# Kernel optimization log

Measured on AMD Instinct MI355X. Metric: run time of the kernel, lower is better.

The kernel has to match this reference:

```python
import jax, jax.numpy as jnp
import numpy as np

B, C, H, W, R = 16, 64, 192, 192, 64

def setup_inputs() -> dict:
    key = jax.random.key(0)
    ks = jax.random.split(key, 8)
    return {
        "X":  jax.random.normal(ks[0], (B, C, H, W), dtype=jnp.float32),
        "p":  jnp.ones((R,), dtype=jnp.float32),  # parameter_r init = ones
        "Wc": jax.random.normal(ks[1], (R, C, C), dtype=jnp.float32) * (1.0 / np.sqrt(C)),
        "bc": jax.random.normal(ks[2], (R, C), dtype=jnp.float32) * 0.01,
        "Wh": jax.random.normal(ks[3], (R, H, H), dtype=jnp.float32) * (1.0 / np.sqrt(H)),
        "bh": jax.random.normal(ks[4], (R, H), dtype=jnp.float32) * 0.01,
        "Ww": jax.random.normal(ks[5], (R, W, W), dtype=jnp.float32) * (1.0 / np.sqrt(W)),
        "bw": jax.random.normal(ks[6], (R, W), dtype=jnp.float32) * 0.01,
    }

def reference(X, p, Wc, bc, Wh, bh, Ww, bw):
    # Global average pools (shared across all r iterations; the torch loop
    # recomputes them redundantly every iteration -- same values).
    cp = X.mean(axis=(2, 3))  # [B,C]  pool over H,W
    hp = X.mean(axis=(1, 3))  # [B,H]  pool over C,W (after permute 0,2,1,3)
    wp = X.mean(axis=(1, 2))  # [B,W]  pool over C,H (after permute 0,3,2,1)
    # Per-iteration 1x1 convs on [*,1,1] == batched affine maps, then sigmoid.
    Cw = jax.nn.sigmoid(jnp.einsum('rdc,bc->rbd', Wc, cp) + bc[:, None, :])  # [R,B,C]
    Hw = jax.nn.sigmoid(jnp.einsum('rdh,bh->rbd', Wh, hp) + bh[:, None, :])  # [R,B,H]
    Ww_ = jax.nn.sigmoid(jnp.einsum('rdw,bw->rbd', Ww, wp) + bw[:, None, :])  # [R,B,W]
    # y = sum_r p[r] * C_weight_r x H_weight_r x W_weight_r  (rank-1-per-axis outer)
    y = jnp.einsum('r,rbc,rbh,rbw->bchw', p, Cw, Hw, Ww_)
    return y * X
```

## Files before the change

kernel.cpp:

```cpp
#include <hip/hip_runtime.h>
#include <hip/hip_bf16.h>
#include <math.h>

#define B_  16
#define C_  64
#define H_  192
#define W_  192
#define R_  64
#define HW_ (H_*W_)

#define OFF_CP  0
#define OFF_HP  1024
#define OFF_WP  4096
#define OFF_MC  7168
#define OFF_HWS 72704
#define OFF_WWS 269312

typedef __attribute__((ext_vector_type(8))) short bf16x8;
typedef __attribute__((ext_vector_type(4))) float f32x4;

static __device__ __forceinline__ short f2bf(float f) {
    unsigned u = __float_as_uint(f);
    unsigned r = u + 0x7fffu + ((u >> 16) & 1u);
    return (short)(r >> 16);
}

__global__ __launch_bounds__(256) void zero_kernel(float* p, int n) {
    int i = blockIdx.x * 256 + threadIdx.x;
    if (i < n) p[i] = 0.f;
}

__global__ __launch_bounds__(256) void pool_kernel(const float* __restrict__ X,
                                                   float* __restrict__ cp,
                                                   float* __restrict__ hp,
                                                   float* __restrict__ wp) {
    int b = blockIdx.x >> 6;
    int c = blockIdx.x & 63;
    int tid = threadIdx.x;
    int wv = tid >> 6, lane = tid & 63;
    const float* base = X + (size_t)(b * C_ + c) * HW_ + wv * 48 * W_;

    __shared__ float rowsum[H_];
    __shared__ float colpart[4][W_];
    __shared__ float cpart[3];

    float col0 = 0.f, col1 = 0.f, col2 = 0.f;
    for (int hh = 0; hh < 48; hh += 4) {
        float x[4][3];
        #pragma unroll
        for (int u = 0; u < 4; ++u) {
            #pragma unroll
            for (int k = 0; k < 3; ++k)
                x[u][k] = base[(hh + u) * W_ + k * 64 + lane];
        }
        #pragma unroll
        for (int u = 0; u < 4; ++u) {
            col0 += x[u][0]; col1 += x[u][1]; col2 += x[u][2];
            float s = x[u][0] + x[u][1] + x[u][2];
            s += __shfl_down(s, 32);
            s += __shfl_down(s, 16);
            s += __shfl_down(s, 8);
            s += __shfl_down(s, 4);
            s += __shfl_down(s, 2);
            s += __shfl_down(s, 1);
            if (lane == 0) rowsum[wv * 48 + hh + u] = s;
        }
    }
    colpart[wv][lane]       = col0;
    colpart[wv][lane + 64]  = col1;
    colpart[wv][lane + 128] = col2;
    __syncthreads();

    const float inv_cw = 1.0f / 12288.0f;
    if (tid < 192) {
        float colv = colpart[0][tid] + colpart[1][tid] + colpart[2][tid] + colpart[3][tid];
        atomicAdd(&wp[b * W_ + tid], colv * inv_cw);
        float rv = rowsum[tid];
        atomicAdd(&hp[b * H_ + tid], rv * inv_cw);
        float s = rv;
        s += __shfl_down(s, 32);
        s += __shfl_down(s, 16);
        s += __shfl_down(s, 8);
        s += __shfl_down(s, 4);
        s += __shfl_down(s, 2);
        s += __shfl_down(s, 1);
        if ((tid & 63) == 0) cpart[tid >> 6] = s;
    }
    __syncthreads();
    if (tid == 0) cp[b * C_ + c] = (cpart[0] + cpart[1] + cpart[2]) * (1.0f / (float)HW_);
}

__global__ __launch_bounds__(256) void affine_sig_kernel(const float* __restrict__ Wsrc,
                                                         const float* __restrict__ bias,
                                                         const float* __restrict__ pool,
                                                         const float* __restrict__ p,
                                                         float* __restrict__ out,
                                                         int D, int K,
                                                         int s_b, int s_d, int s_r) {
    __shared__ float pl[16 * 193];
    int tid = threadIdx.x;
    for (int i = tid; i < 16 * K; i += 256) {
        int bb = i / K, kk = i - bb * K;
        pl[bb * (K + 1) + kk] = pool[i];
    }
    __syncthreads();

    int b  = tid & 15;
    int rl = tid >> 4;
    int row = blockIdx.x * 16 + rl;
    int r = row / D, d = row - r * D;

    const float4* w4 = (const float4*)(Wsrc + (size_t)row * K);
    const float*  pb = &pl[b * (K + 1)];
    float acc = 0.f;
    for (int k4 = 0; k4 < (K >> 2); ++k4) {
        float4 wv = w4[k4];
        int k = k4 << 2;
        acc += wv.x * pb[k] + wv.y * pb[k + 1] + wv.z * pb[k + 2] + wv.w * pb[k + 3];
    }
    acc += bias[row];
    float sgm = 1.0f / (1.0f + expf(-acc));
    if (p) sgm *= p[r];
    out[(size_t)b * s_b + (size_t)d * s_d + (size_t)r * s_r] = sgm;
}

__global__ __launch_bounds__(256) void main_kernel(const float* __restrict__ X,
                                                   const float* __restrict__ Mc,
                                                   const float* __restrict__ Hws,
                                                   const float* __restrict__ Wws,
                                                   float* __restrict__ out) {
    int blk = blockIdx.x;
    int b = blk / 576;
    int rem = blk - b * 576;
    int h = rem / 3;
    int w0 = (rem - h * 3) * 64;
    int tid = threadIdx.x;
    int wv = tid >> 6, lane = tid & 63;
    int m = lane & 15, quad = lane >> 4;
    int c0 = wv * 16;

    const float* McB = Mc + b * (C_ * R_);
    const float* HvB = Hws + ((size_t)b * H_ + h) * R_;
    const float* WwB = Wws + ((size_t)b * W_ + w0) * R_;

    bf16x8 afrag[2];
    float hv[2][8];
    #pragma unroll
    for (int ks = 0; ks < 2; ++ks) {
        const float4* ap = (const float4*)(McB + (c0 + m) * R_ + ks * 32 + quad * 8);
        const float4* hpp = (const float4*)(HvB + ks * 32 + quad * 8);
        float4 a0 = ap[0], a1 = ap[1];
        float4 h0 = hpp[0], h1 = hpp[1];
        afrag[ks][0] = f2bf(a0.x); afrag[ks][1] = f2bf(a0.y);
        afrag[ks][2] = f2bf(a0.z); afrag[ks][3] = f2bf(a0.w);
        afrag[ks][4] = f2bf(a1.x); afrag[ks][5] = f2bf(a1.y);
        afrag[ks][6] = f2bf(a1.z); afrag[ks][7] = f2bf(a1.w);
        hv[ks][0] = h0.x; hv[ks][1] = h0.y; hv[ks][2] = h0.z; hv[ks][3] = h0.w;
        hv[ks][4] = h1.x; hv[ks][5] = h1.y; hv[ks][6] = h1.z; hv[ks][7] = h1.w;
    }

    f32x4 acc[4];
    #pragma unroll
    for (int jt = 0; jt < 4; ++jt) acc[jt] = (f32x4){0.f, 0.f, 0.f, 0.f};

    #pragma unroll
    for (int jt = 0; jt < 4; ++jt) {
        #pragma unroll
        for (int ks = 0; ks < 2; ++ks) {
            const float4* bp = (const float4*)(WwB + (jt * 16 + m) * R_ + ks * 32 + quad * 8);
            float4 b0 = bp[0], b1 = bp[1];
            bf16x8 bfrag;
            bfrag[0] = f2bf(b0.x * hv[ks][0]); bfrag[1] = f2bf(b0.y * hv[ks][1]);
            bfrag[2] = f2bf(b0.z * hv[ks][2]); bfrag[3] = f2bf(b0.w * hv[ks][3]);
            bfrag[4] = f2bf(b1.x * hv[ks][4]); bfrag[5] = f2bf(b1.y * hv[ks][5]);
            bfrag[6] = f2bf(b1.z * hv[ks][6]); bfrag[7] = f2bf(b1.w * hv[ks][7]);
            acc[jt] = __builtin_amdgcn_mfma_f32_16x16x32_bf16(afrag[ks], bfrag, acc[jt], 0, 0, 0);
        }
    }

    size_t pixbase = (size_t)h * W_ + w0 + m;
    #pragma unroll
    for (int jt = 0; jt < 4; ++jt) {
        #pragma unroll
        for (int reg = 0; reg < 4; ++reg) {
            int c = c0 + quad * 4 + reg;
            size_t idx = (size_t)(b * C_ + c) * HW_ + pixbase + jt * 16;
            out[idx] = acc[jt][reg] * X[idx];
        }
    }
}

extern "C" void kernel_launch(void* const* d_in, const int* in_sizes, int n_in,
                              void* d_out, int out_size, void* d_ws, size_t ws_size,
                              hipStream_t stream) {
    const float* X  = (const float*)d_in[0];
    const float* p  = (const float*)d_in[1];
    const float* Wc = (const float*)d_in[2];
    const float* bc = (const float*)d_in[3];
    const float* Wh = (const float*)d_in[4];
    const float* bh = (const float*)d_in[5];
    const float* Ww = (const float*)d_in[6];
    const float* bw = (const float*)d_in[7];
    float* out = (float*)d_out;
    float* ws  = (float*)d_ws;

    float* cp  = ws + OFF_CP;
    float* hp  = ws + OFF_HP;
    float* wp  = ws + OFF_WP;
    float* Mc  = ws + OFF_MC;
    float* Hws = ws + OFF_HWS;
    float* Wws = ws + OFF_WWS;

    zero_kernel<<<24, 256, 0, stream>>>(hp, 6144);

    pool_kernel<<<B_ * C_, 256, 0, stream>>>(X, cp, hp, wp);

    affine_sig_kernel<<<(R_ * C_) / 16, 256, 0, stream>>>(
        Wc, bc, cp, p, Mc, C_, C_, C_ * R_, R_, 1);
    affine_sig_kernel<<<(R_ * H_) / 16, 256, 0, stream>>>(
        Wh, bh, hp, nullptr, Hws, H_, H_, H_ * R_, R_, 1);
    affine_sig_kernel<<<(R_ * W_) / 16, 256, 0, stream>>>(
        Ww, bw, wp, nullptr, Wws, W_, W_, W_ * R_, R_, 1);

    main_kernel<<<B_ * 576, 256, 0, stream>>>(X, Mc, Hws, Wws, out);
}
```

Measured before the change: 403.8 us.

## Transpose MFMA roles for float4 X/out access and merge affine kernels

```diff
diff --git a/kernel.cpp b/kernel.cpp
--- a/kernel.cpp
+++ b/kernel.cpp
@@ -90,14 +90,28 @@
     if (tid == 0) cp[b * C_ + c] = (cpart[0] + cpart[1] + cpart[2]) * (1.0f / (float)HW_);
 }
 
-__global__ __launch_bounds__(256) void affine_sig_kernel(const float* __restrict__ Wsrc,
-                                                         const float* __restrict__ bias,
-                                                         const float* __restrict__ pool,
-                                                         const float* __restrict__ p,
-                                                         float* __restrict__ out,
-                                                         int D, int K,
-                                                         int s_b, int s_d, int s_r) {
+__global__ __launch_bounds__(256) void affine_all_kernel(
+        const float* __restrict__ Wc, const float* __restrict__ bc,
+        const float* __restrict__ Wh, const float* __restrict__ bh,
+        const float* __restrict__ Ww, const float* __restrict__ bw,
+        const float* __restrict__ cp, const float* __restrict__ hp,
+        const float* __restrict__ wp, const float* __restrict__ p,
+        float* __restrict__ Mc, float* __restrict__ Hws, float* __restrict__ Wws) {
     __shared__ float pl[16 * 193];
+    int blk = blockIdx.x;
+    const float *Wsrc, *bias, *pool, *pmul;
+    float* outp;
+    int D, K;
+    if (blk < 256) {
+        Wsrc = Wc; bias = bc; pool = cp; pmul = p; outp = Mc; D = C_; K = C_;
+    } else if (blk < 1024) {
+        blk -= 256;
+        Wsrc = Wh; bias = bh; pool = hp; pmul = nullptr; outp = Hws; D = H_; K = H_;
+    } else {
+        blk -= 1024;
+        Wsrc = Ww; bias = bw; pool = wp; pmul = nullptr; outp = Wws; D = W_; K = W_;
+    }
+
     int tid = threadIdx.x;
     for (int i = tid; i < 16 * K; i += 256) {
         int bb = i / K, kk = i - bb * K;
@@ -107,7 +121,7 @@
 
     int b  = tid & 15;
     int rl = tid >> 4;
-    int row = blockIdx.x * 16 + rl;
+    int row = blk * 16 + rl;
     int r = row / D, d = row - r * D;
 
     const float4* w4 = (const float4*)(Wsrc + (size_t)row * K);
@@ -120,8 +134,11 @@
     }
     acc += bias[row];
     float sgm = 1.0f / (1.0f + expf(-acc));
-    if (p) sgm *= p[r];
-    out[(size_t)b * s_b + (size_t)d * s_d + (size_t)r * s_r] = sgm;
+    if (pmul) sgm *= pmul[r];
+    if (D == C_)
+        outp[(size_t)b * (C_ * R_) + (size_t)d * R_ + r] = sgm;
+    else
+        outp[(size_t)b * (D * R_) + (size_t)d * R_ + r] = sgm;
 }
 
 __global__ __launch_bounds__(256) void main_kernel(const float* __restrict__ X,
@@ -137,56 +154,61 @@
     int tid = threadIdx.x;
     int wv = tid >> 6, lane = tid & 63;
     int m = lane & 15, quad = lane >> 4;
-    int c0 = wv * 16;
 
     const float* McB = Mc + b * (C_ * R_);
     const float* HvB = Hws + ((size_t)b * H_ + h) * R_;
     const float* WwB = Wws + ((size_t)b * W_ + w0) * R_;
 
+    int wbase = w0 + wv * 16 + quad * 4;
+    size_t pixbase = (size_t)h * W_ + wbase;
+    float4 xv[4];
+    #pragma unroll
+    for (int ct = 0; ct < 4; ++ct) {
+        int c = ct * 16 + m;
+        xv[ct] = *(const float4*)(X + (size_t)(b * C_ + c) * HW_ + pixbase);
+    }
+
     bf16x8 afrag[2];
-    float hv[2][8];
     #pragma unroll
     for (int ks = 0; ks < 2; ++ks) {
-        const float4* ap = (const float4*)(McB + (c0 + m) * R_ + ks * 32 + quad * 8);
-        const float4* hpp = (const float4*)(HvB + ks * 32 + quad * 8);
-        float4 a0 = ap[0], a1 = ap[1];
-        float4 h0 = hpp[0], h1 = hpp[1];
-        afrag[ks][0] = f2bf(a0.x); afrag[ks][1] = f2bf(a0.y);
-        afrag[ks][2] = f2bf(a0.z); afrag[ks][3] = f2bf(a0.w);
-        afrag[ks][4] = f2bf(a1.x); afrag[ks][5] = f2bf(a1.y);
-        afrag[ks][6] = f2bf(a1.z); afrag[ks][7] = f2bf(a1.w);
-        hv[ks][0] = h0.x; hv[ks][1] = h0.y; hv[ks][2] = h0.z; hv[ks][3] = h0.w;
-        hv[ks][4] = h1.x; hv[ks][5] = h1.y; hv[ks][6] = h1.z; hv[ks][7] = h1.w;
+        const float4* wp4 = (const float4*)(WwB + (wv * 16 + m) * R_ + ks * 32 + quad * 8);
+        const float4* hp4 = (const float4*)(HvB + ks * 32 + quad * 8);
+        float4 w0v = wp4[0], w1v = wp4[1];
+        float4 h0v = hp4[0], h1v = hp4[1];
+        afrag[ks][0] = f2bf(w0v.x * h0v.x); afrag[ks][1] = f2bf(w0v.y * h0v.y);
+        afrag[ks][2] = f2bf(w0v.z * h0v.z); afrag[ks][3] = f2bf(w0v.w * h0v.w);
+        afrag[ks][4] = f2bf(w1v.x * h1v.x); afrag[ks][5] = f2bf(w1v.y * h1v.y);
+        afrag[ks][6] = f2bf(w1v.z * h1v.z); afrag[ks][7] = f2bf(w1v.w * h1v.w);
     }
 
     f32x4 acc[4];
     #pragma unroll
-    for (int jt = 0; jt < 4; ++jt) acc[jt] = (f32x4){0.f, 0.f, 0.f, 0.f};
-
-    #pragma unroll
-    for (int jt = 0; jt < 4; ++jt) {
+    for (int ct = 0; ct < 4; ++ct) acc[ct] = (f32x4){0.f, 0.f, 0.f, 0.f};
+
+    #pragma unroll
+    for (int ct = 0; ct < 4; ++ct) {
         #pragma unroll
         for (int ks = 0; ks < 2; ++ks) {
-            const float4* bp = (const float4*)(WwB + (jt * 16 + m) * R_ + ks * 32 + quad * 8);
+            const float4* bp = (const float4*)(McB + (ct * 16 + m) * R_ + ks * 32 + quad * 8);
             float4 b0 = bp[0], b1 = bp[1];
             bf16x8 bfrag;
-            bfrag[0] = f2bf(b0.x * hv[ks][0]); bfrag[1] = f2bf(b0.y * hv[ks][1]);
-            bfrag[2] = f2bf(b0.z * hv[ks][2]); bfrag[3] = f2bf(b0.w * hv[ks][3]);
-            bfrag[4] = f2bf(b1.x * hv[ks][4]); bfrag[5] = f2bf(b1.y * hv[ks][5]);
-            bfrag[6] = f2bf(b1.z * hv[ks][6]); bfrag[7] = f2bf(b1.w * hv[ks][7]);
-            acc[jt] = __builtin_amdgcn_mfma_f32_16x16x32_bf16(afrag[ks], bfrag, acc[jt], 0, 0, 0);
+            bfrag[0] = f2bf(b0.x); bfrag[1] = f2bf(b0.y);
+            bfrag[2] = f2bf(b0.z); bfrag[3] = f2bf(b0.w);
+            bfrag[4] = f2bf(b1.x); bfrag[5] = f2bf(b1.y);
+            bfrag[6] = f2bf(b1.z); bfrag[7] = f2bf(b1.w);
+            acc[ct] = __builtin_amdgcn_mfma_f32_16x16x32_bf16(afrag[ks], bfrag, acc[ct], 0, 0, 0);
         }
     }
 
-    size_t pixbase = (size_t)h * W_ + w0 + m;
-    #pragma unroll
-    for (int jt = 0; jt < 4; ++jt) {
-        #pragma unroll
-        for (int reg = 0; reg < 4; ++reg) {
-            int c = c0 + quad * 4 + reg;
-            size_t idx = (size_t)(b * C_ + c) * HW_ + pixbase + jt * 16;
-            out[idx] = acc[jt][reg] * X[idx];
-        }
+    #pragma unroll
+    for (int ct = 0; ct < 4; ++ct) {
+        int c = ct * 16 + m;
+        float4 o;
+        o.x = acc[ct][0] * xv[ct].x;
+        o.y = acc[ct][1] * xv[ct].y;
+        o.z = acc[ct][2] * xv[ct].z;
+        o.w = acc[ct][3] * xv[ct].w;
+        *(float4*)(out + (size_t)(b * C_ + c) * HW_ + pixbase) = o;
     }
 }
 
@@ -215,12 +237,8 @@
 
     pool_kernel<<<B_ * C_, 256, 0, stream>>>(X, cp, hp, wp);
 
-    affine_sig_kernel<<<(R_ * C_) / 16, 256, 0, stream>>>(
-        Wc, bc, cp, p, Mc, C_, C_, C_ * R_, R_, 1);
-    affine_sig_kernel<<<(R_ * H_) / 16, 256, 0, stream>>>(
-        Wh, bh, hp, nullptr, Hws, H_, H_, H_ * R_, R_, 1);
-    affine_sig_kernel<<<(R_ * W_) / 16, 256, 0, stream>>>(
-        Ww, bw, wp, nullptr, Wws, W_, W_, W_ * R_, R_, 1);
+    affine_all_kernel<<<1792, 256, 0, stream>>>(Wc, bc, Wh, bh, Ww, bw,
+                                                cp, hp, wp, p, Mc, Hws, Wws);
 
     main_kernel<<<B_ * 576, 256, 0, stream>>>(X, Mc, Hws, Wws, out);
 }
```

New measurement: 395.2 us. 1.02x faster.
